# Kernel optimization log

Measured on AMD Instinct MI355X. Metric: run time of the kernel, lower is better.

## Reference

```python
import jax, jax.numpy as jnp
import numpy as np

B, HP, WP, C = 64, 16, 32, 512   # batch, rows, cols, cnn_feature_size
H = 512                          # hidden_size
L = 2                            # num_layers
MAXH = 32


def setup_inputs() -> dict:
    key = jax.random.key(0)
    ks = jax.random.split(key, 11)
    s = 0.05  # keep gates out of saturation
    return {
        "features":   jax.random.normal(ks[0], (B, HP, WP, C), jnp.float32),
        "pos_emb_fw": jax.random.normal(ks[1], (MAXH + 1, L * 2 * H), jnp.float32) * s,
        "pos_emb_bw": jax.random.normal(ks[2], (MAXH + 1, L * 2 * H), jnp.float32) * s,
        "Wi_fw": jax.random.normal(ks[3], (L, C, 4 * H), jnp.float32) * s,
        "Wh_fw": jax.random.normal(ks[4], (L, H, 4 * H), jnp.float32) * s,
        "bi_fw": jax.random.normal(ks[5], (L, 4 * H), jnp.float32) * s,
        "bh_fw": jax.random.normal(ks[6], (L, 4 * H), jnp.float32) * s,
        "Wi_bw": jax.random.normal(ks[7], (L, C, 4 * H), jnp.float32) * s,
        "Wh_bw": jax.random.normal(ks[8], (L, H, 4 * H), jnp.float32) * s,
        "bi_bw": jax.random.normal(ks[9], (L, 4 * H), jnp.float32) * s,
        "bh_bw": jax.random.normal(ks[10], (L, 4 * H), jnp.float32) * s,
    }


def _stacked_lstm_scan(xs, h0, c0, Wi, Wh, b):
    """xs: (T, N, C); h0, c0: (L, N, H); returns (T, N, H) top-layer outputs."""
    def step(carry, x_t):
        hs, cs = carry
        inp = x_t
        new_h, new_c = [], []
        for l in range(Wi.shape[0]):
            gates = inp @ Wi[l] + hs[l] @ Wh[l] + b[l]          # (N, 4H)
            i_g, f_g, o_g, g_g = jnp.split(gates, 4, axis=-1)   # gate order as in torch chunk
            c_n = jax.nn.sigmoid(f_g) * cs[l] + jax.nn.sigmoid(i_g) * jnp.tanh(g_g)
            h_n = jax.nn.sigmoid(o_g) * jnp.tanh(c_n)
            new_h.append(h_n); new_c.append(c_n)
            inp = h_n
        return (jnp.stack(new_h), jnp.stack(new_c)), inp
    _, ys = jax.lax.scan(step, (h0, c0), xs)
    return ys


def _init_state(pos_emb, row_idx, n, l, h):
    # pos_emb[row_idx]: (N, L*2*H) laid out as [h_1, c_1, ..., h_L, c_L]
    e = pos_emb[row_idx].reshape(n, l, 2, h)
    return e[:, :, 0].transpose(1, 0, 2), e[:, :, 1].transpose(1, 0, 2)  # (L, N, H) each


def reference(features, pos_emb_fw, pos_emb_bw,
              Wi_fw, Wh_fw, bi_fw, bh_fw,
              Wi_bw, Wh_bw, bi_bw, bh_bw):
    b, hp, wp, c = features.shape
    l, _, h4 = Wi_fw.shape
    h = h4 // 4
    n = b * hp  # rows are independent -> fuse into one scan batch

    # (B, Hp, Wp, C) -> (Wp, B*Hp, C), time-major
    xs = features.transpose(2, 0, 1, 3).reshape(wp, n, c)
    # row index i+1 per flattened (b, row) element
    row_idx = jnp.tile(jnp.arange(1, hp + 1), b)  # (N,)

    h0f, c0f = _init_state(pos_emb_fw, row_idx, n, l, h)
    out_fw = _stacked_lstm_scan(xs, h0f, c0f, Wi_fw, Wh_fw, bi_fw + bh_fw)

    h0b, c0b = _init_state(pos_emb_bw, row_idx, n, l, h)
    out_bw = jnp.flip(
        _stacked_lstm_scan(jnp.flip(xs, 0), h0b, c0b, Wi_bw, Wh_bw, bi_bw + bh_bw), 0)

    ctx = jnp.concatenate([out_fw, out_bw], axis=-1)        # (Wp, N, 2H)
    ctx = ctx.reshape(wp, b, hp, 2 * h).transpose(1, 2, 0, 3)  # (B, Hp, Wp, 2H)
    return ctx.reshape(b, hp * wp, 2 * h)
```

## Files before the change

kernel.cpp:

```cpp
#include <hip/hip_runtime.h>
#include <hip/hip_bf16.h>
#include <stdint.h>

#define B_    64
#define HP_   16
#define WP_   32
#define CH_   512
#define HS_   512
#define NSEQ  1024
#define G4    2048
#define KTOT  1024

typedef __hip_bfloat16 bf16_t;
typedef __bf16 bf16x8 __attribute__((ext_vector_type(8)));
typedef float  f32x4  __attribute__((ext_vector_type(4)));

#define WT_OFF   0
#define XBF_OFF  16777216
#define HBUF_OFF 50331648
#define CBUF_OFF 58720256
#define PB_OFF   67108864
#define HB_ELEMS (2*2*1024*512)

__device__ __forceinline__ float sigf(float x) {
    return 1.0f / (1.0f + __expf(-x));
}
__device__ __forceinline__ float tanhfast(float x) {
    x = fminf(fmaxf(x, -15.0f), 15.0f);
    float e = __expf(-2.0f * x);
    return (1.0f - e) / (1.0f + e);
}

__device__ __forceinline__ void gload16(const bf16_t* g, bf16_t* l) {
    __builtin_amdgcn_global_load_lds(
        (const __attribute__((address_space(1))) void*)g,
        (__attribute__((address_space(3))) void*)l, 16, 0, 0);
}

__global__ void k_prep_w(const float* __restrict__ Wi_fw, const float* __restrict__ Wh_fw,
                         const float* __restrict__ Wi_bw, const float* __restrict__ Wh_bw,
                         bf16_t* __restrict__ Wt) {
    int bxi = blockIdx.x;
    int cb = bxi & 63;
    int kb = (bxi >> 6) & 31;
    int u  = bxi >> 11;
    int l  = u >> 1, dir = u & 1;
    const float* Wi = dir ? Wi_bw : Wi_fw;
    const float* Wh = dir ? Wh_bw : Wh_fw;
    int k0 = kb * 32;
    const float* src = (k0 < 512) ? (Wi + (size_t)l*512*2048 + (size_t)k0*2048)
                                  : (Wh + (size_t)l*512*2048 + (size_t)(k0-512)*2048);
    int jblk = cb >> 2, g = cb & 3;
    int sc0 = g*512 + jblk*32;
    int cp0 = cb * 32;
    __shared__ float ld[32][33];
    int tx = threadIdx.x & 31, ty = threadIdx.x >> 5;
#pragma unroll
    for (int i = 0; i < 4; ++i) {
        int kr = ty + i*8;
        ld[kr][tx] = src[(size_t)kr*2048 + sc0 + tx];
    }
    __syncthreads();
#pragma unroll
    for (int i = 0; i < 4; ++i) {
        int cl = ty + i*8;
        Wt[((size_t)u*G4 + cp0 + cl)*KTOT + k0 + tx] = __float2bfloat16(ld[tx][cl]);
    }
}

__global__ void k_prep_bias(const float* __restrict__ bi_fw, const float* __restrict__ bh_fw,
                            const float* __restrict__ bi_bw, const float* __restrict__ bh_bw,
                            float* __restrict__ pb) {
    int id = blockIdx.x * 256 + threadIdx.x;
    if (id >= 4*G4) return;
    int u = id >> 11, cp = id & 2047;
    int l = u >> 1, dir = u & 1;
    int jblk = cp >> 7, rr = cp & 127, g = rr >> 5, jin = rr & 31;
    int col = g*512 + jblk*32 + jin;
    const float* bi = dir ? bi_bw : bi_fw;
    const float* bh = dir ? bh_bw : bh_fw;
    pb[id] = bi[l*G4 + col] + bh[l*G4 + col];
}

__global__ void k_convert_x(const float* __restrict__ f, bf16_t* __restrict__ xbf) {
    int id = blockIdx.x * 256 + threadIdx.x;
    int c8 = id & 63;
    int t  = (id >> 6) & 31;
    int n  = id >> 11;
    const float* s = f + ((size_t)n*WP_ + t)*CH_ + c8*8;
    bf16_t* d = xbf + ((size_t)t*NSEQ + n)*CH_ + c8*8;
#pragma unroll
    for (int i = 0; i < 8; ++i) d[i] = __float2bfloat16(s[i]);
}

__global__ void k_init_state(const float* __restrict__ pe_fw, const float* __restrict__ pe_bw,
                             bf16_t* __restrict__ hbuf, float* __restrict__ cbuf) {
    int id = blockIdx.x * 256 + threadIdx.x;
    int j = id & 511;
    int n = (id >> 9) & 1023;
    int l = (id >> 19) & 1;
    int dir = id >> 20;
    const float* pe = dir ? pe_bw : pe_fw;
    int rowi = (n & 15) + 1;
    float h = pe[(size_t)rowi*2048 + l*1024 + j];
    float c = pe[(size_t)rowi*2048 + l*1024 + 512 + j];
    int pp = (l == 0) ? 1 : 0;
    hbuf[(size_t)pp*HB_ELEMS + (((size_t)dir*2 + l)*NSEQ + n)*HS_ + j] = __float2bfloat16(h);
    cbuf[(((size_t)dir*2 + l)*NSEQ + n)*HS_ + j] = c;
}

__global__ __launch_bounds__(512, 4) void k_phase(
    int p,
    const bf16_t* __restrict__ xbf,
    const bf16_t* __restrict__ Wt,
    const float*  __restrict__ pb,
    bf16_t* __restrict__ hbuf,
    float*  __restrict__ cbuf,
    float*  __restrict__ out) {

    int bx = blockIdx.x;
    int xcd   = bx & 7;
    int layer = (bx >> 8) & 1;
    int r5    = (bx >> 3) & 31;
    int dir   = r5 & 1;
    int cb    = xcd * 2 + ((r5 >> 1) & 1);
    int rb    = r5 >> 2;
    int u     = layer * 2 + dir;

    if (layer == 0 && p >= WP_) return;
    if (layer == 1 && p < 1)    return;

    int row0 = rb * 128;
    int c0 = cb * 128;

    const bf16_t* hread = hbuf + (size_t)((p + 1) & 1) * HB_ELEMS;
    bf16_t* hwrite      = hbuf + (size_t)(p & 1) * HB_ELEMS;

    const bf16_t* A1;
    const bf16_t* A2;
    int t_out = 0;
    if (layer == 0) {
        int t = dir ? (WP_ - 1 - p) : p;
        A1 = xbf + (size_t)t * NSEQ * CH_;
        A2 = hread + ((size_t)dir*2 + 0) * NSEQ * HS_;
    } else {
        A1 = hread + ((size_t)dir*2 + 0) * NSEQ * HS_;
        A2 = hread + ((size_t)dir*2 + 1) * NSEQ * HS_;
        t_out = dir ? (WP_ - p) : (p - 1);
    }
    const bf16_t* Wu = Wt + (size_t)u * G4 * KTOT;

    __shared__ __align__(16) bf16_t a_lds[2][128*64];
    __shared__ __align__(16) bf16_t b_lds[2][128*64];

    int tid = threadIdx.x;
    int lane = tid & 63;
    int wv = tid >> 6;

    f32x4 acc[8];
#pragma unroll
    for (int n = 0; n < 8; ++n)
        acc[n] = (f32x4){0.f, 0.f, 0.f, 0.f};

    auto STAGE = [&](int kt, int bufi) {
        const bf16_t* Asrc;
        int kloc;
        if (kt < 8) { Asrc = A1; kloc = kt * 64; }
        else        { Asrc = A2; kloc = kt * 64 - 512; }
#pragma unroll
        for (int q = 0; q < 2; ++q) {
            int id = q*512 + tid;
            int r = id >> 3;
            int s = id & 7;
            int kk = ((s ^ (r & 7)) << 3);
            gload16(Asrc + (size_t)(row0 + r)*512 + kloc + kk,
                    a_lds[bufi] + (size_t)(q*512 + (wv << 6)) * 8);
        }
#pragma unroll
        for (int q = 0; q < 2; ++q) {
            int id = q*512 + tid;
            int r = id >> 3;
            int s = id & 7;
            int kk = ((s ^ (r & 7)) << 3);
            gload16(Wu + (size_t)(c0 + r)*KTOT + kt*64 + kk,
                    b_lds[bufi] + (size_t)(q*512 + (wv << 6)) * 8);
        }
    };

    auto COMPUTE = [&](int bufi) {
        const char* ac = (const char*)a_lds[bufi];
        const char* bc = (const char*)b_lds[bufi];
#pragma unroll
        for (int ks = 0; ks < 2; ++ks) {
            int kb = (ks << 5) + ((lane >> 4) << 3);
            bf16x8 av, bv[8];
            {
                int row = (wv << 4) + (lane & 15);
                int byte = row*128 + kb*2;
                byte ^= (row & 7) << 4;
                av = *(const bf16x8*)(ac + byte);
            }
#pragma unroll
            for (int n = 0; n < 8; ++n) {
                int colr = (n << 4) + (lane & 15);
                int byte = colr*128 + kb*2;
                byte ^= (colr & 7) << 4;
                bv[n] = *(const bf16x8*)(bc + byte);
            }
#pragma unroll
            for (int n = 0; n < 8; ++n)
                acc[n] = __builtin_amdgcn_mfma_f32_16x16x32_bf16(av, bv[n], acc[n], 0, 0, 0);
        }
    };

    STAGE(0, 0);
    int cur = 0;
    for (int kt = 0; kt < 15; ++kt) {
        STAGE(kt + 1, cur ^ 1);
        asm volatile("s_waitcnt vmcnt(4)" ::: "memory");
        __builtin_amdgcn_s_barrier();
        COMPUTE(cur);
        __builtin_amdgcn_s_barrier();
        cur ^= 1;
    }
    asm volatile("s_waitcnt vmcnt(0)" ::: "memory");
    __builtin_amdgcn_s_barrier();
    COMPUTE(cur);

    float bias[4][2];
#pragma unroll
    for (int g = 0; g < 4; ++g)
#pragma unroll
        for (int jq = 0; jq < 2; ++jq)
            bias[g][jq] = pb[u*G4 + c0 + g*32 + jq*16 + (lane & 15)];

    float* cptr = cbuf + ((size_t)dir*2 + layer) * NSEQ * HS_;
    bf16_t* hw  = hwrite + ((size_t)dir*2 + layer) * NSEQ * HS_;

#pragma unroll
    for (int jq = 0; jq < 2; ++jq) {
        f32x4 iv = acc[0 + jq];
        f32x4 fv = acc[2 + jq];
        f32x4 ov = acc[4 + jq];
        f32x4 gv = acc[6 + jq];
        int j = cb*32 + jq*16 + (lane & 15);
#pragma unroll
        for (int r = 0; r < 4; ++r) {
            int row = (wv << 4) + ((lane >> 4) << 2) + r;
            int n = row0 + row;
            float ig = sigf(iv[r] + bias[0][jq]);
            float fg = sigf(fv[r] + bias[1][jq]);
            float og = sigf(ov[r] + bias[2][jq]);
            float gg = tanhfast(gv[r] + bias[3][jq]);
            size_t sidx = (size_t)n * HS_ + j;
            float cp = cptr[sidx];
            float cn = fg * cp + ig * gg;
            float hn = og * tanhfast(cn);
            cptr[sidx] = cn;
            hw[sidx] = __float2bfloat16(hn);
            if (layer == 1)
                out[((size_t)n * WP_ + t_out) * (2*HS_) + (size_t)dir*HS_ + j] = hn;
        }
    }
}

extern "C" void kernel_launch(void* const* d_in, const int* in_sizes, int n_in,
                              void* d_out, int out_size, void* d_ws, size_t ws_size,
                              hipStream_t stream) {
    const float* features = (const float*)d_in[0];
    const float* pe_fw = (const float*)d_in[1];
    const float* pe_bw = (const float*)d_in[2];
    const float* Wi_fw = (const float*)d_in[3];
    const float* Wh_fw = (const float*)d_in[4];
    const float* bi_fw = (const float*)d_in[5];
    const float* bh_fw = (const float*)d_in[6];
    const float* Wi_bw = (const float*)d_in[7];
    const float* Wh_bw = (const float*)d_in[8];
    const float* bi_bw = (const float*)d_in[9];
    const float* bh_bw = (const float*)d_in[10];

    char* ws = (char*)d_ws;
    bf16_t* Wt   = (bf16_t*)(ws + WT_OFF);
    bf16_t* xbf  = (bf16_t*)(ws + XBF_OFF);
    bf16_t* hbuf = (bf16_t*)(ws + HBUF_OFF);
    float*  cbuf = (float*)(ws + CBUF_OFF);
    float*  pb   = (float*)(ws + PB_OFF);
    float*  out  = (float*)d_out;

    k_prep_w<<<dim3(8192), dim3(256), 0, stream>>>(Wi_fw, Wh_fw, Wi_bw, Wh_bw, Wt);
    k_prep_bias<<<dim3(32), dim3(256), 0, stream>>>(bi_fw, bh_fw, bi_bw, bh_bw, pb);
    k_convert_x<<<dim3(8192), dim3(256), 0, stream>>>(features, xbf);
    k_init_state<<<dim3(8192), dim3(256), 0, stream>>>(pe_fw, pe_bw, hbuf, cbuf);

    for (int p = 0; p <= WP_; ++p)
        k_phase<<<dim3(512), dim3(512), 0, stream>>>(p, xbf, Wt, pb, hbuf, cbuf, out);
}
```

Baseline: 1.079 ms.

## Replace per-timestep kernel launches with a persistent kernel and grid barrier

Fuses the 33 per-phase LSTM launches into one persistent kernel that loops over phases and synchronizes all blocks with an atomic counter barrier. Bias values are loaded once per block instead of per launch. This removes kernel launch and drain overhead between timesteps. It relies on all 512 blocks being co-resident, and a spinning single-counter barrier adds its own latency and deadlock risk.

New measurement: 2.771 ms. 157% more time.

```diff
diff --git a/kernel.cpp b/kernel.cpp
--- a/kernel.cpp
+++ b/kernel.cpp
@@ -20,6 +20,7 @@
 #define HBUF_OFF 50331648
 #define CBUF_OFF 58720256
 #define PB_OFF   67108864
+#define CNT_OFF  (PB_OFF + 32768)
 #define HB_ELEMS (2*2*1024*512)
 
 __device__ __forceinline__ float sigf(float x) {
@@ -70,8 +71,9 @@
 
 __global__ void k_prep_bias(const float* __restrict__ bi_fw, const float* __restrict__ bh_fw,
                             const float* __restrict__ bi_bw, const float* __restrict__ bh_bw,
-                            float* __restrict__ pb) {
+                            float* __restrict__ pb, uint32_t* __restrict__ cnt) {
     int id = blockIdx.x * 256 + threadIdx.x;
+    if (id == 0) *cnt = 0;
     if (id >= 4*G4) return;
     int u = id >> 11, cp = id & 2047;
     int l = u >> 1, dir = u & 1;
@@ -109,14 +111,14 @@
     cbuf[(((size_t)dir*2 + l)*NSEQ + n)*HS_ + j] = c;
 }
 
-__global__ __launch_bounds__(512, 4) void k_phase(
-    int p,
+__global__ __launch_bounds__(512, 4) void k_persist(
     const bf16_t* __restrict__ xbf,
     const bf16_t* __restrict__ Wt,
     const float*  __restrict__ pb,
     bf16_t* __restrict__ hbuf,
     float*  __restrict__ cbuf,
-    float*  __restrict__ out) {
+    float*  __restrict__ out,
+    uint32_t* __restrict__ cnt) {
 
     int bx = blockIdx.x;
     int xcd   = bx & 7;
@@ -127,27 +129,9 @@
     int rb    = r5 >> 2;
     int u     = layer * 2 + dir;
 
-    if (layer == 0 && p >= WP_) return;
-    if (layer == 1 && p < 1)    return;
-
     int row0 = rb * 128;
     int c0 = cb * 128;
 
-    const bf16_t* hread = hbuf + (size_t)((p + 1) & 1) * HB_ELEMS;
-    bf16_t* hwrite      = hbuf + (size_t)(p & 1) * HB_ELEMS;
-
-    const bf16_t* A1;
-    const bf16_t* A2;
-    int t_out = 0;
-    if (layer == 0) {
-        int t = dir ? (WP_ - 1 - p) : p;
-        A1 = xbf + (size_t)t * NSEQ * CH_;
-        A2 = hread + ((size_t)dir*2 + 0) * NSEQ * HS_;
-    } else {
-        A1 = hread + ((size_t)dir*2 + 0) * NSEQ * HS_;
-        A2 = hread + ((size_t)dir*2 + 1) * NSEQ * HS_;
-        t_out = dir ? (WP_ - p) : (p - 1);
-    }
     const bf16_t* Wu = Wt + (size_t)u * G4 * KTOT;
 
     __shared__ __align__(16) bf16_t a_lds[2][128*64];
@@ -157,110 +141,142 @@
     int lane = tid & 63;
     int wv = tid >> 6;
 
-    f32x4 acc[8];
-#pragma unroll
-    for (int n = 0; n < 8; ++n)
-        acc[n] = (f32x4){0.f, 0.f, 0.f, 0.f};
-
-    auto STAGE = [&](int kt, int bufi) {
-        const bf16_t* Asrc;
-        int kloc;
-        if (kt < 8) { Asrc = A1; kloc = kt * 64; }
-        else        { Asrc = A2; kloc = kt * 64 - 512; }
-#pragma unroll
-        for (int q = 0; q < 2; ++q) {
-            int id = q*512 + tid;
-            int r = id >> 3;
-            int s = id & 7;
-            int kk = ((s ^ (r & 7)) << 3);
-            gload16(Asrc + (size_t)(row0 + r)*512 + kloc + kk,
-                    a_lds[bufi] + (size_t)(q*512 + (wv << 6)) * 8);
-        }
-#pragma unroll
-        for (int q = 0; q < 2; ++q) {
-            int id = q*512 + tid;
-            int r = id >> 3;
-            int s = id & 7;
-            int kk = ((s ^ (r & 7)) << 3);
-            gload16(Wu + (size_t)(c0 + r)*KTOT + kt*64 + kk,
-                    b_lds[bufi] + (size_t)(q*512 + (wv << 6)) * 8);
-        }
-    };
-
-    auto COMPUTE = [&](int bufi) {
-        const char* ac = (const char*)a_lds[bufi];
-        const char* bc = (const char*)b_lds[bufi];
-#pragma unroll
-        for (int ks = 0; ks < 2; ++ks) {
-            int kb = (ks << 5) + ((lane >> 4) << 3);
-            bf16x8 av, bv[8];
-            {
-                int row = (wv << 4) + (lane & 15);
-                int byte = row*128 + kb*2;
-                byte ^= (row & 7) << 4;
-                av = *(const bf16x8*)(ac + byte);
-            }
-#pragma unroll
-            for (int n = 0; n < 8; ++n) {
-                int colr = (n << 4) + (lane & 15);
-                int byte = colr*128 + kb*2;
-                byte ^= (colr & 7) << 4;
-                bv[n] = *(const bf16x8*)(bc + byte);
-            }
-#pragma unroll
-            for (int n = 0; n < 8; ++n)
-                acc[n] = __builtin_amdgcn_mfma_f32_16x16x32_bf16(av, bv[n], acc[n], 0, 0, 0);
-        }
-    };
-
-    STAGE(0, 0);
-    int cur = 0;
-    for (int kt = 0; kt < 15; ++kt) {
-        STAGE(kt + 1, cur ^ 1);
-        asm volatile("s_waitcnt vmcnt(4)" ::: "memory");
-        __builtin_amdgcn_s_barrier();
-        COMPUTE(cur);
-        __builtin_amdgcn_s_barrier();
-        cur ^= 1;
-    }
-    asm volatile("s_waitcnt vmcnt(0)" ::: "memory");
-    __builtin_amdgcn_s_barrier();
-    COMPUTE(cur);
-
     float bias[4][2];
 #pragma unroll
     for (int g = 0; g < 4; ++g)
 #pragma unroll
         for (int jq = 0; jq < 2; ++jq)
             bias[g][jq] = pb[u*G4 + c0 + g*32 + jq*16 + (lane & 15)];
-
     float* cptr = cbuf + ((size_t)dir*2 + layer) * NSEQ * HS_;
-    bf16_t* hw  = hwrite + ((size_t)dir*2 + layer) * NSEQ * HS_;
-
-#pragma unroll
-    for (int jq = 0; jq < 2; ++jq) {
-        f32x4 iv = acc[0 + jq];
-        f32x4 fv = acc[2 + jq];
-        f32x4 ov = acc[4 + jq];
-        f32x4 gv = acc[6 + jq];
-        int j = cb*32 + jq*16 + (lane & 15);
-#pragma unroll
-        for (int r = 0; r < 4; ++r) {
-            int row = (wv << 4) + ((lane >> 4) << 2) + r;
-            int n = row0 + row;
-            float ig = sigf(iv[r] + bias[0][jq]);
-            float fg = sigf(fv[r] + bias[1][jq]);
-            float og = sigf(ov[r] + bias[2][jq]);
-            float gg = tanhfast(gv[r] + bias[3][jq]);
-            size_t sidx = (size_t)n * HS_ + j;
-            float cp = cptr[sidx];
-            float cn = fg * cp + ig * gg;
-            float hn = og * tanhfast(cn);
-            cptr[sidx] = cn;
-            hw[sidx] = __float2bfloat16(hn);
-            if (layer == 1)
-                out[((size_t)n * WP_ + t_out) * (2*HS_) + (size_t)dir*HS_ + j] = hn;
+
+#pragma unroll 1
+    for (int p = 0; p <= WP_; ++p) {
+        bool active = !(layer == 0 && p >= WP_) && !(layer == 1 && p < 1);
+        if (active) {
+            const bf16_t* hread = hbuf + (size_t)((p + 1) & 1) * HB_ELEMS;
+            bf16_t* hwrite      = hbuf + (size_t)(p & 1) * HB_ELEMS;
+
+            const bf16_t* A1;
+            const bf16_t* A2;
+            int t_out = 0;
+            if (layer == 0) {
+                int t = dir ? (WP_ - 1 - p) : p;
+                A1 = xbf + (size_t)t * NSEQ * CH_;
+                A2 = hread + ((size_t)dir*2 + 0) * NSEQ * HS_;
+            } else {
+                A1 = hread + ((size_t)dir*2 + 0) * NSEQ * HS_;
+                A2 = hread + ((size_t)dir*2 + 1) * NSEQ * HS_;
+                t_out = dir ? (WP_ - p) : (p - 1);
+            }
+
+            f32x4 acc[8];
+#pragma unroll
+            for (int n = 0; n < 8; ++n)
+                acc[n] = (f32x4){0.f, 0.f, 0.f, 0.f};
+
+            auto STAGE = [&](int kt, int bufi) {
+                const bf16_t* Asrc;
+                int kloc;
+                if (kt < 8) { Asrc = A1; kloc = kt * 64; }
+                else        { Asrc = A2; kloc = kt * 64 - 512; }
+#pragma unroll
+                for (int q = 0; q < 2; ++q) {
+                    int id = q*512 + tid;
+                    int r = id >> 3;
+                    int s = id & 7;
+                    int kk = ((s ^ (r & 7)) << 3);
+                    gload16(Asrc + (size_t)(row0 + r)*512 + kloc + kk,
+                            a_lds[bufi] + (size_t)(q*512 + (wv << 6)) * 8);
+                }
+#pragma unroll
+                for (int q = 0; q < 2; ++q) {
+                    int id = q*512 + tid;
+                    int r = id >> 3;
+                    int s = id & 7;
+                    int kk = ((s ^ (r & 7)) << 3);
+                    gload16(Wu + (size_t)(c0 + r)*KTOT + kt*64 + kk,
+                            b_lds[bufi] + (size_t)(q*512 + (wv << 6)) * 8);
+                }
+            };
+
+            auto COMPUTE = [&](int bufi) {
+                const char* ac = (const char*)a_lds[bufi];
+                const char* bc = (const char*)b_lds[bufi];
+#pragma unroll
+                for (int ks = 0; ks < 2; ++ks) {
+                    int kb = (ks << 5) + ((lane >> 4) << 3);
+                    bf16x8 av, bv[8];
+                    {
+                        int row = (wv << 4) + (lane & 15);
+                        int byte = row*128 + kb*2;
+                        byte ^= (row & 7) << 4;
+                        av = *(const bf16x8*)(ac + byte);
+                    }
+#pragma unroll
+                    for (int n = 0; n < 8; ++n) {
+                        int colr = (n << 4) + (lane & 15);
+                        int byte = colr*128 + kb*2;
+                        byte ^= (colr & 7) << 4;
+                        bv[n] = *(const bf16x8*)(bc + byte);
+                    }
+#pragma unroll
+                    for (int n = 0; n < 8; ++n)
+                        acc[n] = __builtin_amdgcn_mfma_f32_16x16x32_bf16(av, bv[n], acc[n], 0, 0, 0);
+                }
+            };
+
+            STAGE(0, 0);
+            int cur = 0;
+#pragma unroll 1
+            for (int kt = 0; kt < 15; ++kt) {
+                STAGE(kt + 1, cur ^ 1);
+                asm volatile("s_waitcnt vmcnt(4)" ::: "memory");
+                __builtin_amdgcn_s_barrier();
+                COMPUTE(cur);
+                __builtin_amdgcn_s_barrier();
+                cur ^= 1;
+            }
+            asm volatile("s_waitcnt vmcnt(0)" ::: "memory");
+            __builtin_amdgcn_s_barrier();
+            COMPUTE(cur);
+
+            bf16_t* hw = hwrite + ((size_t)dir*2 + layer) * NSEQ * HS_;
+#pragma unroll
+            for (int jq = 0; jq < 2; ++jq) {
+                f32x4 iv = acc[0 + jq];
+                f32x4 fv = acc[2 + jq];
+                f32x4 ov = acc[4 + jq];
+                f32x4 gv = acc[6 + jq];
+                int j = cb*32 + jq*16 + (lane & 15);
+#pragma unroll
+                for (int r = 0; r < 4; ++r) {
+                    int row = (wv << 4) + ((lane >> 4) << 2) + r;
+                    int n = row0 + row;
+                    float ig = sigf(iv[r] + bias[0][jq]);
+                    float fg = sigf(fv[r] + bias[1][jq]);
+                    float og = sigf(ov[r] + bias[2][jq]);
+                    float gg = tanhfast(gv[r] + bias[3][jq]);
+                    size_t sidx = (size_t)n * HS_ + j;
+                    float cp = cptr[sidx];
+                    float cn = fg * cp + ig * gg;
+                    float hn = og * tanhfast(cn);
+                    cptr[sidx] = cn;
+                    hw[sidx] = __float2bfloat16(hn);
+                    if (layer == 1)
+                        out[((size_t)n * WP_ + t_out) * (2*HS_) + (size_t)dir*HS_ + j] = hn;
+                }
+            }
         }
+
+        __syncthreads();
+        if (tid == 0) {
+            __hip_atomic_fetch_add(cnt, 1u, __ATOMIC_RELEASE, __HIP_MEMORY_SCOPE_AGENT);
+            uint32_t target = (uint32_t)(p + 1) * 512u;
+            while (__hip_atomic_load(cnt, __ATOMIC_RELAXED, __HIP_MEMORY_SCOPE_AGENT) < target)
+                __builtin_amdgcn_s_sleep(8);
+            __hip_atomic_load(cnt, __ATOMIC_ACQUIRE, __HIP_MEMORY_SCOPE_AGENT);
+        }
+        __syncthreads();
     }
 }
 
@@ -285,13 +301,13 @@
     bf16_t* hbuf = (bf16_t*)(ws + HBUF_OFF);
     float*  cbuf = (float*)(ws + CBUF_OFF);
     float*  pb   = (float*)(ws + PB_OFF);
+    uint32_t* cnt = (uint32_t*)(ws + CNT_OFF);
     float*  out  = (float*)d_out;
 
     k_prep_w<<<dim3(8192), dim3(256), 0, stream>>>(Wi_fw, Wh_fw, Wi_bw, Wh_bw, Wt);
-    k_prep_bias<<<dim3(32), dim3(256), 0, stream>>>(bi_fw, bh_fw, bi_bw, bh_bw, pb);
+    k_prep_bias<<<dim3(32), dim3(256), 0, stream>>>(bi_fw, bh_fw, bi_bw, bh_bw, pb, cnt);
     k_convert_x<<<dim3(8192), dim3(256), 0, stream>>>(features, xbf);
     k_init_state<<<dim3(8192), dim3(256), 0, stream>>>(pe_fw, pe_bw, hbuf, cbuf);
 
-    for (int p = 0; p <= WP_; ++p)
-        k_phase<<<dim3(512), dim3(512), 0, stream>>>(p, xbf, Wt, pb, hbuf, cbuf, out);
-}
+    k_persist<<<dim3(512), dim3(512), 0, stream>>>(xbf, Wt, pb, hbuf, cbuf, out, cnt);
+}
```
